# Optimization experiments

Measured on AMD Instinct MI355X. Metric: run time of the kernel, lower is better.

## Reference

```python
import jax, jax.numpy as jnp
import numpy as np

B, H, S, D = 4, 16, 2048, 64


def setup_inputs() -> dict:
    key = jax.random.key(0)
    kq, kk, kv = jax.random.split(key, 3)
    q = jax.random.normal(kq, (B, H, S, D), dtype=jnp.float32)
    k = jax.random.normal(kk, (B, H, S, D), dtype=jnp.float32)
    v = jax.random.normal(kv, (B, H, S, D), dtype=jnp.float32)
    return {"q": q, "k": k, "v": v}


def reference(q, k, v):
    d_k = q.shape[-1]
    scale = 1.0 / jnp.sqrt(jnp.asarray(d_k, dtype=q.dtype))
    # scores: [B, H, S_q, S_k]
    scores = jnp.einsum("bhqd,bhkd->bhqk", q, k) * scale
    attn = jax.nn.softmax(scores, axis=-1)
    out = jnp.einsum("bhqk,bhkd->bhqd", attn, v)
    return out
```

## Files before the change

kernel.cpp:

```cpp
#include <hip/hip_runtime.h>


#define NT 16
#define M0 10.0f

typedef unsigned short u16;
typedef unsigned int   u32;
typedef __bf16 bf16x8 __attribute__((ext_vector_type(8)));
typedef u16    u16x8  __attribute__((ext_vector_type(8)));
typedef u32    u32x4  __attribute__((ext_vector_type(4)));
typedef float  f32x16 __attribute__((ext_vector_type(16)));

__device__ __forceinline__ u16 f2bf(float f) {
    union { float f; u32 u; } x; x.f = f;
    u32 r = x.u + 0x7FFFu + ((x.u >> 16) & 1u);
    return (u16)(r >> 16);
}
__device__ __forceinline__ u32 cvt_pk_bf16(float lo, float hi) {
    u32 r; asm("v_cvt_pk_bf16_f32 %0, %1, %2" : "=v"(r) : "v"(lo), "v"(hi));
    return r;
}
__device__ __forceinline__ float fexp2(float x) {
    float r; asm("v_exp_f32 %0, %1" : "=v"(r) : "v"(x));
    return r;
}

__global__ __launch_bounds__(256)
void prepass_kernel(const float* __restrict__ K, const float* __restrict__ V,
                    u16* __restrict__ Kb, u16* __restrict__ Vt)
{
    __shared__ u16 T[64 * 66];
    const int t   = threadIdx.x;
    const int bh  = blockIdx.x >> 5;
    const int s0  = (blockIdx.x & 31) * 64;
    const int row = t >> 2;
    const int c0  = (t & 3) * 16;

    {
        const float* kp = K + ((size_t)bh * 2048 + s0 + row) * 64 + c0;
        #pragma unroll
        for (int i = 0; i < 2; ++i) {
            float4 a = ((const float4*)kp)[2 * i];
            float4 b = ((const float4*)kp)[2 * i + 1];
            u16x8 o;
            o[0] = f2bf(a.x); o[1] = f2bf(a.y); o[2] = f2bf(a.z); o[3] = f2bf(a.w);
            o[4] = f2bf(b.x); o[5] = f2bf(b.y); o[6] = f2bf(b.z); o[7] = f2bf(b.w);
            *(u16x8*)(Kb + ((size_t)bh * 2048 + s0 + row) * 64 + c0 + 8 * i) = o;
        }
    }
    {
        const float* vp = V + ((size_t)bh * 2048 + s0 + row) * 64 + c0;
        #pragma unroll
        for (int i = 0; i < 4; ++i) {
            float4 a = ((const float4*)vp)[i];
            T[(c0 + 4 * i + 0) * 66 + row] = f2bf(a.x);
            T[(c0 + 4 * i + 1) * 66 + row] = f2bf(a.y);
            T[(c0 + 4 * i + 2) * 66 + row] = f2bf(a.z);
            T[(c0 + 4 * i + 3) * 66 + row] = f2bf(a.w);
        }
    }
    __syncthreads();
    {
        const int d  = t >> 2;
        const int k0 = (t & 3) * 16;
        #pragma unroll
        for (int i = 0; i < 2; ++i) {
            u16x8 o;
            #pragma unroll
            for (int j = 0; j < 8; ++j) o[j] = T[d * 66 + k0 + 8 * i + j];
            *(u16x8*)(Vt + ((size_t)bh * 64 + d) * 2048 + s0 + k0 + 8 * i) = o;
        }
    }
}

__global__ __launch_bounds__(512)
void attn_fwd_kernel(const float* __restrict__ Qg, const u16* __restrict__ Kb,
                     const u16* __restrict__ Vt, float* __restrict__ Og)
{
    __shared__ u16 Klds[2][128 * 64];
    __shared__ u16 Vlds[2][64 * 128];

    const int tid = threadIdx.x;
    const int w   = tid >> 6;
    const int l31 = tid & 31;
    const int hi  = (tid & 63) >> 5;
    const int sw7 = l31 & 7;
    const int m15 = l31 & 15;

    const int id = (blockIdx.x & 7) * 64 + (blockIdx.x >> 3);
    const int bh = id >> 3;
    const int q0 = (id & 7) * 256;
    const int qw = q0 + w * 32;
    const int qr = qw + l31;

    const size_t baseQ = (size_t)bh * 2048 * 64;
    const u16* kg = Kb + (size_t)bh * 2048 * 64;
    const u16* vg = Vt + (size_t)bh * 64 * 2048;

    const float SCL = 0.125f * 1.44269504088896f;
    bf16x8 bq[4];
    #pragma unroll
    for (int dc = 0; dc < 4; ++dc) {
        const float* qp = Qg + baseQ + (size_t)qr * 64 + dc * 16 + hi * 8;
        float4 a = ((const float4*)qp)[0];
        float4 b = ((const float4*)qp)[1];
        u16x8 t;
        t[0] = f2bf(a.x * SCL); t[1] = f2bf(a.y * SCL);
        t[2] = f2bf(a.z * SCL); t[3] = f2bf(a.w * SCL);
        t[4] = f2bf(b.x * SCL); t[5] = f2bf(b.y * SCL);
        t[6] = f2bf(b.z * SCL); t[7] = f2bf(b.w * SCL);
        bq[dc] = __builtin_bit_cast(bf16x8, t);
    }

    int co[4];
    #pragma unroll
    for (int c = 0; c < 4; ++c) co[c] = ((2 * c + hi) ^ sw7) * 8;

    u32x4 onev; onev[0] = 0x3F803F80u; onev[1] = 0x3F803F80u;
    onev[2] = 0x3F803F80u; onev[3] = 0x3F803F80u;
    const bf16x8 bones = __builtin_bit_cast(bf16x8, onev);

    f32x16 acc[2], acc2;
    #pragma unroll
    for (int i = 0; i < 16; ++i) { acc[0][i] = 0.f; acc[1][i] = 0.f; acc2[i] = 0.f; }

    const int r0    = tid >> 3;
    const int ck    = tid & 7;
    const int scolK = ((ck ^ (r0 & 7)) * 8);
    const int vcol0 = ((ck     ^ (r0 & 15)) * 8);
    const int vcol1 = (((ck|8) ^ (r0 & 15)) * 8);
    const u16* kS0 = kg + (size_t)r0 * 64 + scolK;
    const u16* kS1 = kg + (size_t)(r0 + 64) * 64 + scolK;
    const u16* vSr = vg + (size_t)r0 * 2048;

    u16x8 rA, rB, rC, rD;
    auto load_tile = [&](int t) {
        rA = *(const u16x8*)(kS0 + (size_t)t * 8192);
        rB = *(const u16x8*)(kS1 + (size_t)t * 8192);
        rC = *(const u16x8*)(vSr + (size_t)t * 128 + vcol0);
        rD = *(const u16x8*)(vSr + (size_t)t * 128 + vcol1);
    };
    auto write_tile = [&](int t) {
        u16* kd = &Klds[t & 1][r0 * 64 + ck * 8];
        u16* vd = &Vlds[t & 1][r0 * 128 + ck * 8];
        *(u16x8*)kd = rA;
        *(u16x8*)(kd + 4096) = rB;
        *(u16x8*)vd = rC;
        *(u16x8*)(vd + 64) = rD;
    };

    auto sm_pv = [&](f32x16 s, const u16* Vl, int kh) {
        #pragma unroll
        for (int i = 0; i < 16; ++i) s[i] = fexp2(s[i]);
        u32 w0[8];
        #pragma unroll
        for (int a = 0; a < 8; ++a)
            w0[a] = cvt_pk_bf16(s[2 * a], s[2 * a + 1]);
        __builtin_amdgcn_s_setprio(1);
        #pragma unroll
        for (int ki = 0; ki < 2; ++ki) {
            const int ks = kh * 2 + ki, mb = 4 * ki;
            u32 a0 = w0[mb + 0], a2 = w0[mb + 2];
            u32 a1 = w0[mb + 1], a3 = w0[mb + 3];
            asm("v_permlane32_swap_b32 %0, %1" : "+v"(a0), "+v"(a2));
            asm("v_permlane32_swap_b32 %0, %1" : "+v"(a1), "+v"(a3));
            u32x4 fw0; fw0[0] = a0; fw0[1] = a1; fw0[2] = a2; fw0[3] = a3;
            bf16x8 pa = __builtin_bit_cast(bf16x8, fw0);

            const int voff = ((ks * 2 + hi) ^ m15) * 8;
            bf16x8 bv0 = *(const bf16x8*)(Vl + l31 * 128 + voff);
            bf16x8 bv1 = *(const bf16x8*)(Vl + (32 + l31) * 128 + voff);
            acc[0] = __builtin_amdgcn_mfma_f32_32x32x16_bf16(pa, bv0, acc[0], 0, 0, 0);
            acc[1] = __builtin_amdgcn_mfma_f32_32x32x16_bf16(pa, bv1, acc[1], 0, 0, 0);
            acc2   = __builtin_amdgcn_mfma_f32_32x32x16_bf16(pa, bones, acc2, 0, 0, 0);
        }
        __builtin_amdgcn_s_setprio(0);
    };

    auto compute = [&](const u16* Kl, const u16* Vl) {
        #pragma unroll
        for (int p = 0; p < 2; ++p) {
            f32x16 sA, sB;
            #pragma unroll
            for (int i = 0; i < 16; ++i) { sA[i] = -M0; sB[i] = -M0; }
            __builtin_amdgcn_s_setprio(1);
            #pragma unroll
            for (int dc = 0; dc < 4; ++dc) {
                bf16x8 ak0 = *(const bf16x8*)(Kl + (p * 64 + l31) * 64 + co[dc]);
                sA = __builtin_amdgcn_mfma_f32_32x32x16_bf16(ak0, bq[dc], sA, 0, 0, 0);
                bf16x8 ak1 = *(const bf16x8*)(Kl + (p * 64 + 32 + l31) * 64 + co[dc]);
                sB = __builtin_amdgcn_mfma_f32_32x32x16_bf16(ak1, bq[dc], sB, 0, 0, 0);
            }
            __builtin_amdgcn_s_setprio(0);
            sm_pv(sA, Vl, p * 2);
            sm_pv(sB, Vl, p * 2 + 1);
        }
    };

    load_tile(0);
    write_tile(0);
    __syncthreads();
    for (int t = 0; t < NT; ++t) {
        if (t + 1 < NT) load_tile(t + 1);
        compute(Klds[t & 1], Vlds[t & 1]);
        if (t + 1 < NT) {
            write_tile(t + 1);
            __syncthreads();
        }
    }

    #pragma unroll
    for (int r = 0; r < 16; ++r) {
        int cr = (r & 3) + 8 * (r >> 2) + 4 * hi;
        float inv = 1.0f / acc2[r];
        size_t o = baseQ + (size_t)(qw + cr) * 64 + l31;
        Og[o]      = acc[0][r] * inv;
        Og[o + 32] = acc[1][r] * inv;
    }
}

extern "C" void kernel_launch(void* const* d_in, const int* in_sizes, int n_in,
                              void* d_out, int out_size, void* d_ws, size_t ws_size,
                              hipStream_t stream) {
    const float* q = (const float*)d_in[0];
    const float* k = (const float*)d_in[1];
    const float* v = (const float*)d_in[2];
    float* o = (float*)d_out;
    u16* kb = (u16*)d_ws;
    u16* vt = kb + (size_t)64 * 2048 * 64;
    prepass_kernel<<<dim3(2048), dim3(256), 0, stream>>>(k, v, kb, vt);
    attn_fwd_kernel<<<dim3(512), dim3(512), 0, stream>>>(q, kb, vt, o);
}
```

Measured before the change: 99.21 us.

## Software-pipeline softmax exp with the deferred PV MFMA of the previous chunk

Splits each 128-key tile into four 32-key chunks and defers each chunk's P·V MFMAs by one step. The QK MFMAs of the current chunk and the PV of the previous chunk can then overlap the exp and bf16 packing. Pending probabilities are carried across tiles in registers, with a final drain after the loop. This is meant to hide transcendental latency behind matrix work, at the cost of extra live registers and more complex buffer-lifetime reasoning.

```diff
diff --git a/kernel.cpp b/kernel.cpp
--- a/kernel.cpp
+++ b/kernel.cpp
@@ -149,19 +149,18 @@
         *(u16x8*)(vd + 64) = rD;
     };
 
-    auto sm_pv = [&](f32x16 s, const u16* Vl, int kh) {
-        #pragma unroll
-        for (int i = 0; i < 16; ++i) s[i] = fexp2(s[i]);
-        u32 w0[8];
-        #pragma unroll
-        for (int a = 0; a < 8; ++a)
-            w0[a] = cvt_pk_bf16(s[2 * a], s[2 * a + 1]);
+    u32 pw[8];
+    #pragma unroll
+    for (int a = 0; a < 8; ++a) pw[a] = 0u;
+    const u16* Vp = Vlds[0];
+
+    auto pv_pend = [&](const u16* Vl, int qprev) {
         __builtin_amdgcn_s_setprio(1);
         #pragma unroll
         for (int ki = 0; ki < 2; ++ki) {
-            const int ks = kh * 2 + ki, mb = 4 * ki;
-            u32 a0 = w0[mb + 0], a2 = w0[mb + 2];
-            u32 a1 = w0[mb + 1], a3 = w0[mb + 3];
+            const int ks = qprev * 2 + ki, mb = 4 * ki;
+            u32 a0 = pw[mb + 0], a2 = pw[mb + 2];
+            u32 a1 = pw[mb + 1], a3 = pw[mb + 3];
             asm("v_permlane32_swap_b32 %0, %1" : "+v"(a0), "+v"(a2));
             asm("v_permlane32_swap_b32 %0, %1" : "+v"(a1), "+v"(a3));
             u32x4 fw0; fw0[0] = a0; fw0[1] = a1; fw0[2] = a2; fw0[3] = a3;
@@ -177,37 +176,43 @@
         __builtin_amdgcn_s_setprio(0);
     };
 
-    auto compute = [&](const u16* Kl, const u16* Vl) {
-        #pragma unroll
-        for (int p = 0; p < 2; ++p) {
-            f32x16 sA, sB;
-            #pragma unroll
-            for (int i = 0; i < 16; ++i) { sA[i] = -M0; sB[i] = -M0; }
-            __builtin_amdgcn_s_setprio(1);
-            #pragma unroll
-            for (int dc = 0; dc < 4; ++dc) {
-                bf16x8 ak0 = *(const bf16x8*)(Kl + (p * 64 + l31) * 64 + co[dc]);
-                sA = __builtin_amdgcn_mfma_f32_32x32x16_bf16(ak0, bq[dc], sA, 0, 0, 0);
-                bf16x8 ak1 = *(const bf16x8*)(Kl + (p * 64 + 32 + l31) * 64 + co[dc]);
-                sB = __builtin_amdgcn_mfma_f32_32x32x16_bf16(ak1, bq[dc], sB, 0, 0, 0);
-            }
-            __builtin_amdgcn_s_setprio(0);
-            sm_pv(sA, Vl, p * 2);
-            sm_pv(sB, Vl, p * 2 + 1);
-        }
-    };
-
     load_tile(0);
     write_tile(0);
     __syncthreads();
     for (int t = 0; t < NT; ++t) {
         if (t + 1 < NT) load_tile(t + 1);
-        compute(Klds[t & 1], Vlds[t & 1]);
+        const u16* Kl = Klds[t & 1];
+        const u16* Vl = Vlds[t & 1];
+
+        #pragma unroll
+        for (int q = 0; q < 4; ++q) {
+            f32x16 s;
+            #pragma unroll
+            for (int i = 0; i < 16; ++i) s[i] = -M0;
+            __builtin_amdgcn_s_setprio(1);
+            #pragma unroll
+            for (int dc = 0; dc < 4; ++dc) {
+                bf16x8 ak = *(const bf16x8*)(Kl + (q * 32 + l31) * 64 + co[dc]);
+                s = __builtin_amdgcn_mfma_f32_32x32x16_bf16(ak, bq[dc], s, 0, 0, 0);
+            }
+            __builtin_amdgcn_s_setprio(0);
+
+            pv_pend(Vp, (q + 3) & 3);
+
+            #pragma unroll
+            for (int i = 0; i < 16; ++i) s[i] = fexp2(s[i]);
+            #pragma unroll
+            for (int a = 0; a < 8; ++a)
+                pw[a] = cvt_pk_bf16(s[2 * a], s[2 * a + 1]);
+            Vp = Vl;
+        }
+
         if (t + 1 < NT) {
             write_tile(t + 1);
             __syncthreads();
         }
     }
+    pv_pend(Vp, 3);
 
     #pragma unroll
     for (int r = 0; r < 16; ++r) {
```

After: 96.83 us, median of 2. 2.4% less time.
